# Optimization experiments

Hardware: AMD Instinct MI355X
Metric: run time of the kernel (lower is better)

## Reference

```python
import jax, jax.numpy as jnp
import numpy as np


def setup_inputs() -> dict:
    key = jax.random.key(0)
    k1, k2 = jax.random.split(key)
    B, S, D, T = 64, 1024, 512, 2048
    x = jax.random.normal(k1, (B, S, D), dtype=jnp.float32)
    durations = jax.random.randint(k2, (B, S), 0, 8, dtype=jnp.int32)
    return {"x": x, "durations": durations, "max_length": T}


def reference(x, durations, max_length):
    # x: [B, S, D]; durations: [B, S] (non-negative ints); max_length: static int.
    # Equivalent to per-sample repeat_interleave + pad_sequence + slice to max_length,
    # assuming max(sum(durations, axis=1)) >= max_length (true by construction here,
    # matching torch's min(lengths.max(), max_length) == max_length).
    S = x.shape[1]
    cum = jnp.cumsum(durations, axis=1)          # [B, S] exclusive boundary cumsum
    t = jnp.arange(max_length)                   # [T]
    # idx[b, t] = source phoneme index producing output frame t
    idx = jax.vmap(lambda c: jnp.searchsorted(c, t, side='right'))(cum)  # [B, T]
    lengths = cum[:, -1]                         # [B] total frames per sample
    mask = t[None, :] >= lengths[:, None]        # [B, T] True = padding (matches torch ~(<))
    idx = jnp.minimum(idx, S - 1)                # clip out-of-range indices (masked anyway)
    out = jnp.take_along_axis(x, idx[:, :, None], axis=1)  # [B, T, D] gather
    out = jnp.where(mask[:, :, None], jnp.zeros((), x.dtype), out)  # pad value 0
    return out, mask
```

## Files before the change

### kernel.cpp

```cpp
#include <hip/hip_runtime.h>

constexpr int B = 64;
constexpr int S = 1024;
constexpr int D = 512;
constexpr int T = 2048;
constexpr int FPB = 64;
constexpr int CHUNKS = T / FPB;

__global__ __launch_bounds__(256) void length_regulator_kernel(
    const float* __restrict__ x,
    const int*   __restrict__ dur,
    float*       __restrict__ out,
    float*       __restrict__ mask)
{
    __shared__ int cum[S];
    __shared__ int part[256];
    __shared__ int fidx[FPB];
    __shared__ int s_len;

    const int tid   = threadIdx.x;
    const int chunk = blockIdx.x;
    const int b     = blockIdx.y;

    const int4 d4 = ((const int4*)(dur + b * S))[tid];
    const int p0 = d4.x;
    const int p1 = p0 + d4.y;
    const int p2 = p1 + d4.z;
    const int p3 = p2 + d4.w;

    part[tid] = p3;
    __syncthreads();
    int incl = p3;
    for (int off = 1; off < 256; off <<= 1) {
        const int v = (tid >= off) ? part[tid - off] : 0;
        __syncthreads();
        incl += v;
        part[tid] = incl;
        __syncthreads();
    }
    const int excl = incl - p3;
    cum[4 * tid + 0] = excl + p0;
    cum[4 * tid + 1] = excl + p1;
    cum[4 * tid + 2] = excl + p2;
    cum[4 * tid + 3] = excl + p3;
    if (tid == 255) s_len = excl + p3;
    __syncthreads();
    const int len = s_len;

    const int t0 = chunk * FPB;
    if (tid < FPB) {
        const int t = t0 + tid;
        int id = -1;
        if (t < len) {
            int lo = 0, hi = S;
            while (lo < hi) {
                const int mid = (lo + hi) >> 1;
                if (cum[mid] > t) hi = mid; else lo = mid + 1;
            }
            id = lo;
        }
        fidx[tid] = id;
        mask[b * T + t] = (id < 0) ? 1.0f : 0.0f;
    }
    __syncthreads();

    const int sub = tid >> 7;
    const int j   = tid & 127;
    const float4* xb = (const float4*)(x + (size_t)b * S * D);
    float4*       ob = (float4*)(out + ((size_t)b * T + t0) * D);

    #pragma unroll 8
    for (int it = 0; it < FPB / 2; ++it) {
        const int tl = it * 2 + sub;
        const int id = fidx[tl];
        float4 v;
        if (id >= 0) v = xb[(size_t)id * (D / 4) + j];
        else         v = make_float4(0.f, 0.f, 0.f, 0.f);
        ob[(size_t)tl * (D / 4) + j] = v;
    }
}

extern "C" void kernel_launch(void* const* d_in, const int* in_sizes, int n_in,
                              void* d_out, int out_size, void* d_ws, size_t ws_size,
                              hipStream_t stream) {
    const float* x   = (const float*)d_in[0];
    const int*   dur = (const int*)d_in[1];
    float* out  = (float*)d_out;
    float* mask = out + (size_t)B * T * D;

    dim3 grid(CHUNKS, B);
    length_regulator_kernel<<<grid, 256, 0, stream>>>(x, dur, out, mask);
}
```

Measured before the change: 366.4 us.

## Split cumsum scan into separate kernel and use nontemporal stores in copy

The per-batch duration scan and binary search move into their own kernel, launched once per batch, which writes frame indices to workspace. Before, all 32 chunk blocks of a batch each recomputed the same scan. The copy kernel then just reads the indices and gathers rows, writing output with nontemporal stores to avoid polluting cache. This adds a second launch and a round trip through global memory for the indices.

```diff
diff --git a/kernel.cpp b/kernel.cpp
--- a/kernel.cpp
+++ b/kernel.cpp
@@ -7,20 +7,18 @@
 constexpr int FPB = 64;
 constexpr int CHUNKS = T / FPB;
 
-__global__ __launch_bounds__(256) void length_regulator_kernel(
-    const float* __restrict__ x,
-    const int*   __restrict__ dur,
-    float*       __restrict__ out,
-    float*       __restrict__ mask)
+typedef float floatx4 __attribute__((ext_vector_type(4)));
+
+__global__ __launch_bounds__(256) void lr_scan_kernel(
+    const int* __restrict__ dur,
+    int*       __restrict__ fidx,
+    float*     __restrict__ mask)
 {
     __shared__ int cum[S];
     __shared__ int part[256];
-    __shared__ int fidx[FPB];
-    __shared__ int s_len;
 
-    const int tid   = threadIdx.x;
-    const int chunk = blockIdx.x;
-    const int b     = blockIdx.y;
+    const int tid = threadIdx.x;
+    const int b   = blockIdx.x;
 
     const int4 d4 = ((const int4*)(dur + b * S))[tid];
     const int p0 = d4.x;
@@ -43,13 +41,12 @@
     cum[4 * tid + 1] = excl + p1;
     cum[4 * tid + 2] = excl + p2;
     cum[4 * tid + 3] = excl + p3;
-    if (tid == 255) s_len = excl + p3;
     __syncthreads();
-    const int len = s_len;
+    const int len = cum[S - 1];
 
-    const int t0 = chunk * FPB;
-    if (tid < FPB) {
-        const int t = t0 + tid;
+    #pragma unroll
+    for (int k = 0; k < T / 256; ++k) {
+        const int t = k * 256 + tid;
         int id = -1;
         if (t < len) {
             int lo = 0, hi = S;
@@ -59,24 +56,38 @@
             }
             id = lo;
         }
-        fidx[tid] = id;
-        mask[b * T + t] = (id < 0) ? 1.0f : 0.0f;
+        fidx[b * T + t] = id;
+        __builtin_nontemporal_store((id < 0) ? 1.0f : 0.0f, &mask[b * T + t]);
     }
+}
+
+__global__ __launch_bounds__(256) void lr_copy_kernel(
+    const float* __restrict__ x,
+    const int*   __restrict__ fidx,
+    float*       __restrict__ out)
+{
+    __shared__ int fr[FPB];
+
+    const int tid   = threadIdx.x;
+    const int chunk = blockIdx.x;
+    const int b     = blockIdx.y;
+    const int t0    = chunk * FPB;
+
+    if (tid < FPB) fr[tid] = fidx[b * T + t0 + tid];
     __syncthreads();
 
     const int sub = tid >> 7;
     const int j   = tid & 127;
-    const float4* xb = (const float4*)(x + (size_t)b * S * D);
-    float4*       ob = (float4*)(out + ((size_t)b * T + t0) * D);
+    const floatx4* xb = (const floatx4*)(x + (size_t)b * S * D);
+    floatx4*       ob = (floatx4*)(out + ((size_t)b * T + t0) * D);
 
     #pragma unroll 8
     for (int it = 0; it < FPB / 2; ++it) {
         const int tl = it * 2 + sub;
-        const int id = fidx[tl];
-        float4 v;
+        const int id = fr[tl];
+        floatx4 v = (floatx4)(0.f);
         if (id >= 0) v = xb[(size_t)id * (D / 4) + j];
-        else         v = make_float4(0.f, 0.f, 0.f, 0.f);
-        ob[(size_t)tl * (D / 4) + j] = v;
+        __builtin_nontemporal_store(v, &ob[(size_t)tl * (D / 4) + j]);
     }
 }
 
@@ -87,7 +98,9 @@
     const int*   dur = (const int*)d_in[1];
     float* out  = (float*)d_out;
     float* mask = out + (size_t)B * T * D;
+    int*   fidx = (int*)d_ws;
 
+    lr_scan_kernel<<<B, 256, 0, stream>>>(dur, fidx, mask);
     dim3 grid(CHUNKS, B);
-    length_regulator_kernel<<<grid, 256, 0, stream>>>(x, dur, out, mask);
+    lr_copy_kernel<<<grid, 256, 0, stream>>>(x, fidx, out);
 }
```

Result: no change. 367.8 us (+0.4%).
